# Kernel tuning notes

Hardware: AMD Instinct MI355X
Metric: run time of the kernel (lower is better)

## Reference

```python
import jax, jax.numpy as jnp
import numpy as np
from functools import partial

STRIDES = (8, 16, 32)
SIZES = ((80, 80), (40, 40), (20, 20))
NUM_CLASSES = 80
NMS_THR = 0.65
SCORE_THR = 0.01
MAX_DET = 100  # fixed-size NMS output (padded; validity = scores > 0)


def setup_inputs() -> dict:
    key = jax.random.key(0)
    ks = jax.random.split(key, 9)
    B = 32
    out = {}
    for i, (h, w) in enumerate(SIZES):
        out[f"cls{i}"] = jax.random.normal(ks[3 * i], (B, NUM_CLASSES, h, w), jnp.float32)
        out[f"reg{i}"] = jax.random.normal(ks[3 * i + 1], (B, 4, h, w), jnp.float32)
        out[f"obj{i}"] = jax.random.normal(ks[3 * i + 2], (B, 1, h, w), jnp.float32)
    return out


def _grid_points():
    # MlvlPointGenerator.grid_priors(with_stride=True), offset=0: (x, y, stride, stride)
    pts = []
    for (h, w), s in zip(SIZES, STRIDES):
        xs = jnp.arange(w, dtype=jnp.float32) * s
        ys = jnp.arange(h, dtype=jnp.float32) * s
        xx, yy = jnp.meshgrid(xs, ys)  # [h, w], x varies fastest -> matches NHWC flatten
        st = jnp.full((h * w,), float(s), jnp.float32)
        pts.append(jnp.stack([xx.ravel(), yy.ravel(), st, st], axis=-1))
    return jnp.concatenate(pts, axis=0)  # [A, 4]


def _flatten(t, c):
    # [N, C, H, W] -> [N, H*W, C]  (permute(0,2,3,1).reshape)
    return t.transpose(0, 2, 3, 1).reshape(t.shape[0], -1, c)


def _decode(points, reg):
    # YOLOXBBoxDecoder: center = pred_xy * stride + point, wh = exp(pred_wh) * stride
    stride = points[:, 2:]                       # [A, 2]
    xys = reg[..., :2] * stride + points[:, :2]  # [B, A, 2]
    whs = jnp.exp(reg[..., 2:]) * stride         # [B, A, 2]
    return jnp.concatenate([xys - whs * 0.5, xys + whs * 0.5], axis=-1)  # x1y1x2y2


def _iou_one_vs_all(b, boxes):
    # b: [4], boxes: [A, 4]
    tl = jnp.maximum(b[:2], boxes[:, :2])
    br = jnp.minimum(b[2:], boxes[:, 2:])
    wh = jnp.clip(br - tl, 0.0)
    inter = wh[:, 0] * wh[:, 1]
    a1 = (b[2] - b[0]) * (b[3] - b[1])
    a2 = (boxes[:, 2] - boxes[:, 0]) * (boxes[:, 3] - boxes[:, 1])
    return inter / (a1 + a2 - inter + 1e-6)


def _nms_image(boxes, cls_scores, objectness):
    # boxes [A,4], cls_scores [A,C] (post-sigmoid), objectness [A] (post-sigmoid)
    max_scores = jnp.max(cls_scores, axis=1)
    labels = jnp.argmax(cls_scores, axis=1)
    scores = max_scores * objectness
    live = jnp.where(scores >= SCORE_THR, scores, -jnp.inf)  # score_thr filter

    # batched_nms: offset boxes per class so boxes of different labels never overlap
    offset = jax.lax.stop_gradient(jnp.max(jnp.abs(boxes)) + 1.0)
    boxes_off = jax.lax.stop_gradient(boxes) + labels.astype(boxes.dtype)[:, None] * offset

    def body(i, state):
        live, keep, kscores = state
        best = jnp.argmax(live)
        kscores = kscores.at[i].set(live[best])
        keep = keep.at[i].set(best)
        iou = _iou_one_vs_all(boxes_off[best], boxes_off)
        live = jnp.where(iou > NMS_THR, -jnp.inf, live)
        live = live.at[best].set(-jnp.inf)
        return live, keep, kscores

    keep0 = jnp.zeros((MAX_DET,), jnp.int32)
    ks0 = jnp.full((MAX_DET,), -jnp.inf, boxes.dtype)
    _, keep, kscores = jax.lax.fori_loop(0, MAX_DET, body, (live, keep0, ks0))

    valid = kscores > -jnp.inf
    out_boxes = jnp.where(valid[:, None], boxes[keep], 0.0)
    out_scores = jnp.where(valid, scores[keep], 0.0)
    out_labels = jnp.where(valid, labels[keep], -1)
    return out_boxes, out_scores, out_labels, valid


def _forward(cls0, cls1, cls2, reg0, reg1, reg2, obj0, obj1, obj2):
    B = cls0.shape[0]
    flat_cls = jax.nn.sigmoid(jnp.concatenate([_flatten(c, NUM_CLASSES) for c in (cls0, cls1, cls2)], axis=1))
    flat_reg = jnp.concatenate([_flatten(r, 4) for r in (reg0, reg1, reg2)], axis=1)
    flat_obj = jax.nn.sigmoid(jnp.concatenate([_flatten(o, 1) for o in (obj0, obj1, obj2)], axis=1))[..., 0]
    points = _grid_points()
    boxes = _decode(points, flat_reg)  # [B, A, 4]
    return jax.vmap(_nms_image)(boxes, flat_cls, flat_obj)


@jax.jit
def reference(cls0, cls1, cls2, reg0, reg1, reg2, obj0, obj1, obj2):
    return _forward(cls0, cls1, cls2, reg0, reg1, reg2, obj0, obj1, obj2)
```

## Files before the change

kernel.cpp:

```cpp
#include <hip/hip_runtime.h>
#include <cmath>

typedef unsigned int uint;
typedef unsigned long long ull;

#define BATCH 32
#define NA 8400
#define NC 80
#define MAXDET 100
#define NMSTHR 0.65f
#define SCTHR 0.01f
#define NEG_INF (-INFINITY)

#define NT 1024
#define NW (NT / 64)
#define EPT 9
#define NBINS 4096
#define CAP 512

__device__ __forceinline__ float stable_sigmoid(float x) {
    if (x >= 0.f) return 1.f / (1.f + expf(-x));
    float e = expf(x);
    return e / (1.f + e);
}

template<int HW, int W, int S>
__device__ __forceinline__ void decode_one(
    const float* __restrict__ cls, const float* __restrict__ reg,
    const float* __restrict__ obj, int b, int p, size_t gidx,
    float4* __restrict__ wboxes, float* __restrict__ wscores, int* __restrict__ wlabels)
{
    const float* cbase = cls + (size_t)b * NC * HW + p;

    float mq[4]; int lq[4];
    #pragma unroll
    for (int q = 0; q < 4; ++q) { mq[q] = NEG_INF; lq[q] = 0; }
    #pragma unroll
    for (int q = 0; q < 4; ++q) {
        #pragma unroll
        for (int c2 = 0; c2 < 20; ++c2) {
            int c = q * 20 + c2;
            float v = cbase[(size_t)c * HW];
            if (v > mq[q]) { mq[q] = v; lq[q] = c; }
        }
    }
    float maxv = mq[0]; int lab = lq[0];
    #pragma unroll
    for (int q = 1; q < 4; ++q)
        if (mq[q] > maxv) { maxv = mq[q]; lab = lq[q]; }

    const float* rb = reg + (size_t)b * 4 * HW + p;
    float r0 = rb[0];
    float r1 = rb[HW];
    float r2 = rb[2 * (size_t)HW];
    float r3 = rb[3 * (size_t)HW];
    float ov = obj[(size_t)b * HW + p];

    int y = p / W;
    int x = p - y * W;
    float score = stable_sigmoid(maxv) * stable_sigmoid(ov);
    float cx = r0 * (float)S + (float)x * (float)S;
    float cy = r1 * (float)S + (float)y * (float)S;
    float bw = expf(r2) * (float)S;
    float bh = expf(r3) * (float)S;

    wboxes[gidx]  = make_float4(cx - bw * 0.5f, cy - bh * 0.5f,
                                cx + bw * 0.5f, cy + bh * 0.5f);
    wscores[gidx] = score;
    wlabels[gidx] = lab;
}

__global__ __launch_bounds__(256) void decode_kernel(
    const float* __restrict__ cls0, const float* __restrict__ reg0, const float* __restrict__ obj0,
    const float* __restrict__ cls1, const float* __restrict__ reg1, const float* __restrict__ obj1,
    const float* __restrict__ cls2, const float* __restrict__ reg2, const float* __restrict__ obj2,
    float4* __restrict__ wboxes, float* __restrict__ wscores, int* __restrict__ wlabels)
{
    int gid = blockIdx.x * blockDim.x + threadIdx.x;
    int b = gid / NA;
    int j = gid - b * NA;
    size_t gidx = (size_t)gid;

    if (j < 6400)
        decode_one<6400, 80, 8>(cls0, reg0, obj0, b, j, gidx, wboxes, wscores, wlabels);
    else if (j < 8000)
        decode_one<1600, 40, 16>(cls1, reg1, obj1, b, j - 6400, gidx, wboxes, wscores, wlabels);
    else
        decode_one<400, 20, 32>(cls2, reg2, obj2, b, j - 8000, gidx, wboxes, wscores, wlabels);
}

__global__ __launch_bounds__(NT) void nms_kernel(
    const float4* __restrict__ wboxes, const float* __restrict__ wscores,
    const int* __restrict__ wlabels, float* __restrict__ out)
{
    int b = blockIdx.x;
    int t = threadIdx.x;
    int lane = t & 63;
    int wv = t >> 6;
    const float4* boxes  = wboxes  + (size_t)b * NA;
    const float*  scores = wscores + (size_t)b * NA;
    const int*    labels = wlabels + (size_t)b * NA;

    __shared__ uint  s_keys[NA];
    __shared__ uint  s_hist[NBINS];
    __shared__ uint  s_cum[NBINS + 1];
    __shared__ uint  s_wsum[NW];
    __shared__ ull   s_skey[CAP];
    __shared__ float s_kbox[MAXDET][4];
    __shared__ float s_ka1[MAXDET];
    __shared__ int   s_kidx[MAXDET];
    __shared__ float s_kscr[MAXDET];
    __shared__ int   s_klab[MAXDET];
    __shared__ float s_red[NW];
    __shared__ float s_off;
    __shared__ int   s_kept, s_winlo, s_winhi, s_nsel;

    float m = 0.f;
    #pragma unroll
    for (int w = 0; w < EPT; ++w) {
        int e = t + w * NT;
        if (e < NA) {
            float4 v = boxes[e];
            m = fmaxf(m, fmaxf(fmaxf(fabsf(v.x), fabsf(v.y)),
                               fmaxf(fabsf(v.z), fabsf(v.w))));
        }
    }
    #pragma unroll
    for (int o = 32; o >= 1; o >>= 1) m = fmaxf(m, __shfl_xor(m, o));
    if (lane == 0) s_red[wv] = m;
    __syncthreads();
    if (t == 0) {
        float mm = 0.f;
        for (int w = 0; w < NW; ++w) mm = fmaxf(mm, s_red[w]);
        s_off = mm + 1.f;
        s_kept = 0;
        s_winlo = 0;
    }

    #pragma unroll
    for (int w = 0; w < EPT; ++w) {
        int e = t + w * NT;
        if (e < NA) {
            float sc = scores[e];
            s_keys[e] = (sc >= SCTHR) ? ~__float_as_uint(sc) : 0xFFFFFFFFu;
        }
    }
    for (int i = t; i < NBINS; i += NT) s_hist[i] = 0;
    __syncthreads();
    float off = s_off;
    #pragma unroll
    for (int w = 0; w < EPT; ++w) {
        int e = t + w * NT;
        if (e < NA) {
            uint k = s_keys[e];
            if (k != 0xFFFFFFFFu) atomicAdd(&s_hist[k >> 20], 1u);
        }
    }
    __syncthreads();

    uint l0 = s_hist[4 * t], l1 = s_hist[4 * t + 1],
         l2 = s_hist[4 * t + 2], l3 = s_hist[4 * t + 3];
    uint L = l0 + l1 + l2 + l3;
    uint ls = L;
    #pragma unroll
    for (int o = 1; o < 64; o <<= 1) {
        uint v = __shfl_up(ls, o);
        if (lane >= o) ls += v;
    }
    if (lane == 63) s_wsum[wv] = ls;
    __syncthreads();
    if (t < NW) {
        uint v = s_wsum[t];
        uint vs = v;
        #pragma unroll
        for (int o = 1; o < NW; o <<= 1) {
            uint u = __shfl_up(vs, o);
            if ((t & 63) >= o) vs += u;
        }
        s_wsum[t] = vs - v;
    }
    __syncthreads();
    uint base = s_wsum[wv] + (ls - L);
    s_cum[4 * t]     = base;
    s_cum[4 * t + 1] = base + l0;
    s_cum[4 * t + 2] = base + l0 + l1;
    s_cum[4 * t + 3] = base + l0 + l1 + l2;
    if (t == NT - 1) s_cum[NBINS] = base + L;

    for (;;) {
        __syncthreads();
        int kept = s_kept, winlo = s_winlo;
        uint remaining = s_cum[NBINS] - s_cum[winlo];
        if (kept >= MAXDET || winlo >= NBINS || remaining == 0u) break;
        if (t == 0) { s_winhi = winlo + 1; s_nsel = 0; }
        if (t < CAP) s_skey[t] = ~0ull;
        __syncthreads();
        uint cl = s_cum[winlo];
        #pragma unroll
        for (int q = 0; q < 4; ++q) {
            int i = t + q * NT;
            if (i >= winlo && i < NBINS && (s_cum[i + 1] - cl) <= (uint)CAP)
                atomicMax(&s_winhi, i + 1);
        }
        __syncthreads();
        int winhi = s_winhi;

        #pragma unroll
        for (int w = 0; w < EPT; ++w) {
            int e = t + w * NT;
            bool q = false;
            uint k = 0;
            if (e < NA) {
                k = s_keys[e];
                if (k != 0xFFFFFFFFu) {
                    int bin = (int)(k >> 20);
                    q = (bin >= winlo && bin < winhi);
                }
            }
            ull mask = __ballot(q);
            if (mask) {
                int leader = __ffsll(mask) - 1;
                int pbase = 0;
                if (lane == leader) pbase = atomicAdd(&s_nsel, __popcll(mask));
                pbase = __shfl(pbase, leader);
                if (q) {
                    int pos = pbase + __popcll(mask & ((1ull << lane) - 1ull));
                    if (pos < CAP) s_skey[pos] = ((ull)k << 32) | (uint)e;
                }
            }
        }
        __syncthreads();
        int nsel = s_nsel; if (nsel > CAP) nsel = CAP;

        for (int k2 = 2; k2 <= CAP; k2 <<= 1) {
            for (int j = k2 >> 1; j > 0; j >>= 1) {
                __syncthreads();
                if (t < CAP) {
                    int p = t ^ j;
                    if (p > t) {
                        ull a = s_skey[t], bb = s_skey[p];
                        bool up = ((t & k2) == 0);
                        if ((a > bb) == up) { s_skey[t] = bb; s_skey[p] = a; }
                    }
                }
            }
        }
        __syncthreads();

        if (t < 64) {
            int kept2 = s_kept;
            for (int cb = 0; cb < nsel && kept2 < MAXDET; cb += 64) {
                int ci = cb + lane;
                ull sk = (ci < nsel) ? s_skey[ci] : ~0ull;
                bool has = (sk != ~0ull);
                int idx = 0, lab = 0;
                float sc = 0.f, c0 = 0.f, c1 = 0.f, c2 = 0.f, c3 = 0.f, ca = 0.f;
                if (has) {
                    idx = (int)(sk & 0xFFFFFFFFull);
                    sc  = __uint_as_float(~(uint)(sk >> 32));
                    float4 rb = boxes[idx];
                    lab = labels[idx];
                    float lo = (float)lab * off;
                    c0 = rb.x + lo; c1 = rb.y + lo; c2 = rb.z + lo; c3 = rb.w + lo;
                    ca = (c2 - c0) * (c3 - c1);
                    for (int q = 0; q < kept2; ++q) {
                        float tlx = fmaxf(s_kbox[q][0], c0);
                        float tly = fmaxf(s_kbox[q][1], c1);
                        float brx = fminf(s_kbox[q][2], c2);
                        float bry = fminf(s_kbox[q][3], c3);
                        float ww = fmaxf(brx - tlx, 0.f);
                        float hh = fmaxf(bry - tly, 0.f);
                        float inter = ww * hh;
                        float iou = inter / (s_ka1[q] + ca - inter + 1e-6f);
                        if (iou > NMSTHR) { has = false; break; }
                    }
                }
                ull am = __ballot(has);
                while (am && kept2 < MAXDET) {
                    int f = __ffsll(am) - 1;
                    float f0 = __shfl(c0, f), f1 = __shfl(c1, f);
                    float f2 = __shfl(c2, f), f3 = __shfl(c3, f);
                    float fa = __shfl(ca, f);
                    int   fidx = __shfl(idx, f);
                    int   flab = __shfl(lab, f);
                    float fsc  = __shfl(sc, f);
                    if (lane == 0) {
                        s_kbox[kept2][0] = f0; s_kbox[kept2][1] = f1;
                        s_kbox[kept2][2] = f2; s_kbox[kept2][3] = f3;
                        s_ka1[kept2] = fa; s_kidx[kept2] = fidx;
                        s_kscr[kept2] = fsc; s_klab[kept2] = flab;
                    }
                    kept2++;
                    if (lane == f) has = false;
                    if (has) {
                        float tlx = fmaxf(f0, c0), tly = fmaxf(f1, c1);
                        float brx = fminf(f2, c2), bry = fminf(f3, c3);
                        float ww = fmaxf(brx - tlx, 0.f), hh = fmaxf(bry - tly, 0.f);
                        float inter = ww * hh;
                        float iou = inter / (fa + ca - inter + 1e-6f);
                        if (iou > NMSTHR) has = false;
                    }
                    am = __ballot(has);
                }
            }
            if (lane == 0) s_kept = kept2;
        }
        __syncthreads();
        if (t == 0) s_winlo = s_winhi;
    }
    __syncthreads();

    if (t < MAXDET) {
        int kept = s_kept;
        float4 obx = make_float4(0.f, 0.f, 0.f, 0.f);
        float osc = 0.f, olab = -1.f, oval = 0.f;
        if (t < kept) {
            int idx = s_kidx[t];
            obx  = boxes[idx];
            osc  = s_kscr[t];
            olab = (float)s_klab[t];
            oval = 1.f;
        }
        float* ob = out + ((size_t)b * MAXDET + t) * 4;
        ob[0] = obx.x; ob[1] = obx.y; ob[2] = obx.z; ob[3] = obx.w;
        out[BATCH * MAXDET * 4 + b * MAXDET + t] = osc;
        out[BATCH * MAXDET * 5 + b * MAXDET + t] = olab;
        out[BATCH * MAXDET * 6 + b * MAXDET + t] = oval;
    }
}

extern "C" void kernel_launch(void* const* d_in, const int* in_sizes, int n_in,
                              void* d_out, int out_size, void* d_ws, size_t ws_size,
                              hipStream_t stream) {
    const float* cls0 = (const float*)d_in[0];
    const float* reg0 = (const float*)d_in[1];
    const float* obj0 = (const float*)d_in[2];
    const float* cls1 = (const float*)d_in[3];
    const float* reg1 = (const float*)d_in[4];
    const float* obj1 = (const float*)d_in[5];
    const float* cls2 = (const float*)d_in[6];
    const float* reg2 = (const float*)d_in[7];
    const float* obj2 = (const float*)d_in[8];

    char* ws = (char*)d_ws;
    float4* wboxes  = (float4*)ws;
    float*  wscores = (float*)(ws + (size_t)BATCH * NA * sizeof(float4));
    int*    wlabels = (int*)(ws + (size_t)BATCH * NA * (sizeof(float4) + sizeof(float)));

    int total = BATCH * NA;
    decode_kernel<<<total / 256, 256, 0, stream>>>(
        cls0, reg0, obj0, cls1, reg1, obj1, cls2, reg2, obj2,
        wboxes, wscores, wlabels);

    nms_kernel<<<BATCH, NT, 0, stream>>>(wboxes, wscores, wlabels, (float*)d_out);
}
```

Measured before the change: 178.2 us.

## Move score keys, histogram and max-abs reduction into decode kernel; register bitonic sort

The decode kernel now also computes the sort keys, a per-image score histogram built with global atomics, and the per-image max absolute box coordinate. These three values were previously recomputed by a single 1024-thread block per image in the NMS kernel, whose prologue was a serial pass over 8400 boxes; moving them to the widely parallel decode kernel removes that pass. The bitonic sort now keeps keys in registers and uses wave shuffles for strides below 64, so block barriers are only needed for the larger strides. In exchange it adds a memset launch, contended global atomics on the histograms, and per-element global reads of the keys in the NMS selection loop.

```diff
diff --git a/kernel.cpp b/kernel.cpp
--- a/kernel.cpp
+++ b/kernel.cpp
@@ -27,8 +27,8 @@
 template<int HW, int W, int S>
 __device__ __forceinline__ void decode_one(
     const float* __restrict__ cls, const float* __restrict__ reg,
-    const float* __restrict__ obj, int b, int p, size_t gidx,
-    float4* __restrict__ wboxes, float* __restrict__ wscores, int* __restrict__ wlabels)
+    const float* __restrict__ obj, int b, int p,
+    float4* box, float* score, int* lab_out)
 {
     const float* cbase = cls + (size_t)b * NC * HW + p;
 
@@ -58,51 +58,72 @@
 
     int y = p / W;
     int x = p - y * W;
-    float score = stable_sigmoid(maxv) * stable_sigmoid(ov);
+    float sc = stable_sigmoid(maxv) * stable_sigmoid(ov);
     float cx = r0 * (float)S + (float)x * (float)S;
     float cy = r1 * (float)S + (float)y * (float)S;
     float bw = expf(r2) * (float)S;
     float bh = expf(r3) * (float)S;
 
-    wboxes[gidx]  = make_float4(cx - bw * 0.5f, cy - bh * 0.5f,
-                                cx + bw * 0.5f, cy + bh * 0.5f);
-    wscores[gidx] = score;
-    wlabels[gidx] = lab;
+    *box = make_float4(cx - bw * 0.5f, cy - bh * 0.5f,
+                       cx + bw * 0.5f, cy + bh * 0.5f);
+    *score = sc;
+    *lab_out = lab;
 }
 
 __global__ __launch_bounds__(256) void decode_kernel(
     const float* __restrict__ cls0, const float* __restrict__ reg0, const float* __restrict__ obj0,
     const float* __restrict__ cls1, const float* __restrict__ reg1, const float* __restrict__ obj1,
     const float* __restrict__ cls2, const float* __restrict__ reg2, const float* __restrict__ obj2,
-    float4* __restrict__ wboxes, float* __restrict__ wscores, int* __restrict__ wlabels)
+    float4* __restrict__ wboxes, int* __restrict__ wlabels, uint* __restrict__ wkeys,
+    uint* __restrict__ whist, uint* __restrict__ wmaxabs)
 {
     int gid = blockIdx.x * blockDim.x + threadIdx.x;
     int b = gid / NA;
     int j = gid - b * NA;
-    size_t gidx = (size_t)gid;
-
+    int lane = threadIdx.x & 63;
+
+    float4 box; float score; int lab;
     if (j < 6400)
-        decode_one<6400, 80, 8>(cls0, reg0, obj0, b, j, gidx, wboxes, wscores, wlabels);
+        decode_one<6400, 80, 8>(cls0, reg0, obj0, b, j, &box, &score, &lab);
     else if (j < 8000)
-        decode_one<1600, 40, 16>(cls1, reg1, obj1, b, j - 6400, gidx, wboxes, wscores, wlabels);
+        decode_one<1600, 40, 16>(cls1, reg1, obj1, b, j - 6400, &box, &score, &lab);
     else
-        decode_one<400, 20, 32>(cls2, reg2, obj2, b, j - 8000, gidx, wboxes, wscores, wlabels);
+        decode_one<400, 20, 32>(cls2, reg2, obj2, b, j - 8000, &box, &score, &lab);
+
+    wboxes[gid]  = box;
+    wlabels[gid] = lab;
+    uint key = (score >= SCTHR) ? ~__float_as_uint(score) : 0xFFFFFFFFu;
+    wkeys[gid] = key;
+    if (key != 0xFFFFFFFFu) atomicAdd(&whist[(size_t)b * NBINS + (key >> 20)], 1u);
+
+    float m = fmaxf(fmaxf(fabsf(box.x), fabsf(box.y)),
+                    fmaxf(fabsf(box.z), fabsf(box.w)));
+    int b0 = __shfl(b, 0);
+    float mh = (b == b0) ? m : 0.f;
+    float ml = (b == b0) ? 0.f : m;
+    #pragma unroll
+    for (int o = 32; o >= 1; o >>= 1) {
+        mh = fmaxf(mh, __shfl_xor(mh, o));
+        ml = fmaxf(ml, __shfl_xor(ml, o));
+    }
+    if (lane == 0) atomicMax(&wmaxabs[b0], __float_as_uint(mh));
+    int b63 = __shfl(b, 63);
+    if (lane == 63 && b63 != b0) atomicMax(&wmaxabs[b63], __float_as_uint(ml));
 }
 
 __global__ __launch_bounds__(NT) void nms_kernel(
-    const float4* __restrict__ wboxes, const float* __restrict__ wscores,
-    const int* __restrict__ wlabels, float* __restrict__ out)
+    const float4* __restrict__ wboxes, const int* __restrict__ wlabels,
+    const uint* __restrict__ wkeys, const uint* __restrict__ whist,
+    const uint* __restrict__ wmaxabs, float* __restrict__ out)
 {
     int b = blockIdx.x;
     int t = threadIdx.x;
     int lane = t & 63;
     int wv = t >> 6;
     const float4* boxes  = wboxes  + (size_t)b * NA;
-    const float*  scores = wscores + (size_t)b * NA;
     const int*    labels = wlabels + (size_t)b * NA;
-
-    __shared__ uint  s_keys[NA];
-    __shared__ uint  s_hist[NBINS];
+    const uint*   keys   = wkeys   + (size_t)b * NA;
+
     __shared__ uint  s_cum[NBINS + 1];
     __shared__ uint  s_wsum[NW];
     __shared__ ull   s_skey[CAP];
@@ -111,55 +132,12 @@
     __shared__ int   s_kidx[MAXDET];
     __shared__ float s_kscr[MAXDET];
     __shared__ int   s_klab[MAXDET];
-    __shared__ float s_red[NW];
-    __shared__ float s_off;
     __shared__ int   s_kept, s_winlo, s_winhi, s_nsel;
 
-    float m = 0.f;
-    #pragma unroll
-    for (int w = 0; w < EPT; ++w) {
-        int e = t + w * NT;
-        if (e < NA) {
-            float4 v = boxes[e];
-            m = fmaxf(m, fmaxf(fmaxf(fabsf(v.x), fabsf(v.y)),
-                               fmaxf(fabsf(v.z), fabsf(v.w))));
-        }
-    }
-    #pragma unroll
-    for (int o = 32; o >= 1; o >>= 1) m = fmaxf(m, __shfl_xor(m, o));
-    if (lane == 0) s_red[wv] = m;
-    __syncthreads();
-    if (t == 0) {
-        float mm = 0.f;
-        for (int w = 0; w < NW; ++w) mm = fmaxf(mm, s_red[w]);
-        s_off = mm + 1.f;
-        s_kept = 0;
-        s_winlo = 0;
-    }
-
-    #pragma unroll
-    for (int w = 0; w < EPT; ++w) {
-        int e = t + w * NT;
-        if (e < NA) {
-            float sc = scores[e];
-            s_keys[e] = (sc >= SCTHR) ? ~__float_as_uint(sc) : 0xFFFFFFFFu;
-        }
-    }
-    for (int i = t; i < NBINS; i += NT) s_hist[i] = 0;
-    __syncthreads();
-    float off = s_off;
-    #pragma unroll
-    for (int w = 0; w < EPT; ++w) {
-        int e = t + w * NT;
-        if (e < NA) {
-            uint k = s_keys[e];
-            if (k != 0xFFFFFFFFu) atomicAdd(&s_hist[k >> 20], 1u);
-        }
-    }
-    __syncthreads();
-
-    uint l0 = s_hist[4 * t], l1 = s_hist[4 * t + 1],
-         l2 = s_hist[4 * t + 2], l3 = s_hist[4 * t + 3];
+    float off = __uint_as_float(wmaxabs[b]) + 1.f;
+
+    uint4 h = ((const uint4*)(whist + (size_t)b * NBINS))[t];
+    uint l0 = h.x, l1 = h.y, l2 = h.z, l3 = h.w;
     uint L = l0 + l1 + l2 + l3;
     uint ls = L;
     #pragma unroll
@@ -168,6 +146,7 @@
         if (lane >= o) ls += v;
     }
     if (lane == 63) s_wsum[wv] = ls;
+    if (t == 0) { s_kept = 0; s_winlo = 0; }
     __syncthreads();
     if (t < NW) {
         uint v = s_wsum[t];
@@ -211,7 +190,7 @@
             bool q = false;
             uint k = 0;
             if (e < NA) {
-                k = s_keys[e];
+                k = keys[e];
                 if (k != 0xFFFFFFFFu) {
                     int bin = (int)(k >> 20);
                     q = (bin >= winlo && bin < winhi);
@@ -232,19 +211,28 @@
         __syncthreads();
         int nsel = s_nsel; if (nsel > CAP) nsel = CAP;
 
+        ull k = (t < CAP) ? s_skey[t] : ~0ull;
         for (int k2 = 2; k2 <= CAP; k2 <<= 1) {
             for (int j = k2 >> 1; j > 0; j >>= 1) {
-                __syncthreads();
-                if (t < CAP) {
-                    int p = t ^ j;
-                    if (p > t) {
-                        ull a = s_skey[t], bb = s_skey[p];
-                        bool up = ((t & k2) == 0);
-                        if ((a > bb) == up) { s_skey[t] = bb; s_skey[p] = a; }
+                if (j >= 64) {
+                    if (t < CAP) s_skey[t] = k;
+                    __syncthreads();
+                    if (t < CAP) {
+                        ull kp = s_skey[t ^ j];
+                        bool low = (t & j) == 0;
+                        bool up  = (t & k2) == 0;
+                        k = ((k < kp) == (low == up)) ? k : kp;
                     }
+                    __syncthreads();
+                } else if (t < CAP) {
+                    ull kp = __shfl_xor(k, j);
+                    bool low = (t & j) == 0;
+                    bool up  = (t & k2) == 0;
+                    k = ((k < kp) == (low == up)) ? k : kp;
                 }
             }
         }
+        if (t < CAP) s_skey[t] = k;
         __syncthreads();
 
         if (t < 64) {
@@ -343,14 +331,20 @@
     const float* obj2 = (const float*)d_in[8];
 
     char* ws = (char*)d_ws;
+    size_t nBA = (size_t)BATCH * NA;
     float4* wboxes  = (float4*)ws;
-    float*  wscores = (float*)(ws + (size_t)BATCH * NA * sizeof(float4));
-    int*    wlabels = (int*)(ws + (size_t)BATCH * NA * (sizeof(float4) + sizeof(float)));
+    int*    wlabels = (int*)(ws + nBA * 16);
+    uint*   wkeys   = (uint*)(ws + nBA * 20);
+    uint*   whist   = (uint*)(ws + nBA * 24);
+    uint*   wmaxabs = (uint*)(ws + nBA * 24 + (size_t)BATCH * NBINS * 4);
+
+    hipMemsetAsync(whist, 0, (size_t)BATCH * NBINS * 4 + BATCH * 4, stream);
 
     int total = BATCH * NA;
     decode_kernel<<<total / 256, 256, 0, stream>>>(
         cls0, reg0, obj0, cls1, reg1, obj1, cls2, reg2, obj2,
-        wboxes, wscores, wlabels);
-
-    nms_kernel<<<BATCH, NT, 0, stream>>>(wboxes, wscores, wlabels, (float*)d_out);
-}
+        wboxes, wlabels, wkeys, whist, wmaxabs);
+
+    nms_kernel<<<BATCH, NT, 0, stream>>>(wboxes, wlabels, wkeys, whist, wmaxabs,
+                                         (float*)d_out);
+}
```

After: 222.5 us. 24.9% more time.

## Split class argmax across 4 lanes, precompute sort keys, shuffle-based bitonic sort

Applied to the files above, without the earlier changes.

The decode kernel now assigns four threads per anchor. Each thread scans 20 classes and the partial maxima are merged with cross-lane shuffles, which raises parallelism and the number of memory loads in flight. Decode also writes the score-derived sort keys directly, so the NMS kernel no longer stages keys in shared memory and rereads them from global memory instead. The bitonic sort keeps keys in registers and uses wave shuffles for strides below 64, cutting barriers and shared-memory traffic. Tie handling in the argmax uses the lowest class index, which matches argmax semantics.

```diff
diff --git a/kernel.cpp b/kernel.cpp
--- a/kernel.cpp
+++ b/kernel.cpp
@@ -25,83 +25,83 @@
 }
 
 template<int HW, int W, int S>
-__device__ __forceinline__ void decode_one(
+__device__ __forceinline__ void decode4(
     const float* __restrict__ cls, const float* __restrict__ reg,
-    const float* __restrict__ obj, int b, int p, size_t gidx,
-    float4* __restrict__ wboxes, float* __restrict__ wscores, int* __restrict__ wlabels)
+    const float* __restrict__ obj, int b, int p, int q, int ag,
+    float4* __restrict__ wboxes, int* __restrict__ wlabels, uint* __restrict__ wkeys)
 {
-    const float* cbase = cls + (size_t)b * NC * HW + p;
-
-    float mq[4]; int lq[4];
-    #pragma unroll
-    for (int q = 0; q < 4; ++q) { mq[q] = NEG_INF; lq[q] = 0; }
-    #pragma unroll
-    for (int q = 0; q < 4; ++q) {
-        #pragma unroll
-        for (int c2 = 0; c2 < 20; ++c2) {
-            int c = q * 20 + c2;
-            float v = cbase[(size_t)c * HW];
-            if (v > mq[q]) { mq[q] = v; lq[q] = c; }
-        }
-    }
-    float maxv = mq[0]; int lab = lq[0];
-    #pragma unroll
-    for (int q = 1; q < 4; ++q)
-        if (mq[q] > maxv) { maxv = mq[q]; lab = lq[q]; }
-
-    const float* rb = reg + (size_t)b * 4 * HW + p;
-    float r0 = rb[0];
-    float r1 = rb[HW];
-    float r2 = rb[2 * (size_t)HW];
-    float r3 = rb[3 * (size_t)HW];
-    float ov = obj[(size_t)b * HW + p];
-
-    int y = p / W;
-    int x = p - y * W;
-    float score = stable_sigmoid(maxv) * stable_sigmoid(ov);
-    float cx = r0 * (float)S + (float)x * (float)S;
-    float cy = r1 * (float)S + (float)y * (float)S;
-    float bw = expf(r2) * (float)S;
-    float bh = expf(r3) * (float)S;
-
-    wboxes[gidx]  = make_float4(cx - bw * 0.5f, cy - bh * 0.5f,
-                                cx + bw * 0.5f, cy + bh * 0.5f);
-    wscores[gidx] = score;
-    wlabels[gidx] = lab;
+    const float* cbase = cls + (size_t)b * NC * HW + (size_t)(q * 20) * HW + p;
+    float v[20];
+    #pragma unroll
+    for (int i = 0; i < 20; ++i) v[i] = cbase[(size_t)i * HW];
+    float m = v[0]; int c = 0;
+    #pragma unroll
+    for (int i = 1; i < 20; ++i)
+        if (v[i] > m) { m = v[i]; c = i; }
+    c += q * 20;
+
+    #pragma unroll
+    for (int o = 1; o <= 2; o <<= 1) {
+        float om = __shfl_xor(m, o);
+        int   oc = __shfl_xor(c, o);
+        if (om > m || (om == m && oc < c)) { m = om; c = oc; }
+    }
+
+    if (q == 0) {
+        const float* rb = reg + (size_t)b * 4 * HW + p;
+        float r0 = rb[0];
+        float r1 = rb[HW];
+        float r2 = rb[2 * (size_t)HW];
+        float r3 = rb[3 * (size_t)HW];
+        float ov = obj[(size_t)b * HW + p];
+
+        int y = p / W;
+        int x = p - y * W;
+        float sc = stable_sigmoid(m) * stable_sigmoid(ov);
+        float cx = r0 * (float)S + (float)x * (float)S;
+        float cy = r1 * (float)S + (float)y * (float)S;
+        float bw = expf(r2) * (float)S;
+        float bh = expf(r3) * (float)S;
+
+        wboxes[ag]  = make_float4(cx - bw * 0.5f, cy - bh * 0.5f,
+                                  cx + bw * 0.5f, cy + bh * 0.5f);
+        wlabels[ag] = c;
+        wkeys[ag]   = (sc >= SCTHR) ? ~__float_as_uint(sc) : 0xFFFFFFFFu;
+    }
 }
 
 __global__ __launch_bounds__(256) void decode_kernel(
     const float* __restrict__ cls0, const float* __restrict__ reg0, const float* __restrict__ obj0,
     const float* __restrict__ cls1, const float* __restrict__ reg1, const float* __restrict__ obj1,
     const float* __restrict__ cls2, const float* __restrict__ reg2, const float* __restrict__ obj2,
-    float4* __restrict__ wboxes, float* __restrict__ wscores, int* __restrict__ wlabels)
+    float4* __restrict__ wboxes, int* __restrict__ wlabels, uint* __restrict__ wkeys)
 {
     int gid = blockIdx.x * blockDim.x + threadIdx.x;
-    int b = gid / NA;
-    int j = gid - b * NA;
-    size_t gidx = (size_t)gid;
+    int ag = gid >> 2;
+    int q  = gid & 3;
+    int b = ag / NA;
+    int j = ag - b * NA;
 
     if (j < 6400)
-        decode_one<6400, 80, 8>(cls0, reg0, obj0, b, j, gidx, wboxes, wscores, wlabels);
+        decode4<6400, 80, 8>(cls0, reg0, obj0, b, j, q, ag, wboxes, wlabels, wkeys);
     else if (j < 8000)
-        decode_one<1600, 40, 16>(cls1, reg1, obj1, b, j - 6400, gidx, wboxes, wscores, wlabels);
+        decode4<1600, 40, 16>(cls1, reg1, obj1, b, j - 6400, q, ag, wboxes, wlabels, wkeys);
     else
-        decode_one<400, 20, 32>(cls2, reg2, obj2, b, j - 8000, gidx, wboxes, wscores, wlabels);
+        decode4<400, 20, 32>(cls2, reg2, obj2, b, j - 8000, q, ag, wboxes, wlabels, wkeys);
 }
 
 __global__ __launch_bounds__(NT) void nms_kernel(
-    const float4* __restrict__ wboxes, const float* __restrict__ wscores,
-    const int* __restrict__ wlabels, float* __restrict__ out)
+    const float4* __restrict__ wboxes, const int* __restrict__ wlabels,
+    const uint* __restrict__ wkeys, float* __restrict__ out)
 {
     int b = blockIdx.x;
     int t = threadIdx.x;
     int lane = t & 63;
     int wv = t >> 6;
     const float4* boxes  = wboxes  + (size_t)b * NA;
-    const float*  scores = wscores + (size_t)b * NA;
     const int*    labels = wlabels + (size_t)b * NA;
-
-    __shared__ uint  s_keys[NA];
+    const uint*   keys   = wkeys   + (size_t)b * NA;
+
     __shared__ uint  s_hist[NBINS];
     __shared__ uint  s_cum[NBINS + 1];
     __shared__ uint  s_wsum[NW];
@@ -128,35 +128,24 @@
     #pragma unroll
     for (int o = 32; o >= 1; o >>= 1) m = fmaxf(m, __shfl_xor(m, o));
     if (lane == 0) s_red[wv] = m;
+    for (int i = t; i < NBINS; i += NT) s_hist[i] = 0;
+    if (t == 0) { s_kept = 0; s_winlo = 0; }
     __syncthreads();
     if (t == 0) {
         float mm = 0.f;
         for (int w = 0; w < NW; ++w) mm = fmaxf(mm, s_red[w]);
         s_off = mm + 1.f;
-        s_kept = 0;
-        s_winlo = 0;
-    }
-
+    }
     #pragma unroll
     for (int w = 0; w < EPT; ++w) {
         int e = t + w * NT;
         if (e < NA) {
-            float sc = scores[e];
-            s_keys[e] = (sc >= SCTHR) ? ~__float_as_uint(sc) : 0xFFFFFFFFu;
-        }
-    }
-    for (int i = t; i < NBINS; i += NT) s_hist[i] = 0;
+            uint k = keys[e];
+            if (k != 0xFFFFFFFFu) atomicAdd(&s_hist[k >> 20], 1u);
+        }
+    }
     __syncthreads();
     float off = s_off;
-    #pragma unroll
-    for (int w = 0; w < EPT; ++w) {
-        int e = t + w * NT;
-        if (e < NA) {
-            uint k = s_keys[e];
-            if (k != 0xFFFFFFFFu) atomicAdd(&s_hist[k >> 20], 1u);
-        }
-    }
-    __syncthreads();
 
     uint l0 = s_hist[4 * t], l1 = s_hist[4 * t + 1],
          l2 = s_hist[4 * t + 2], l3 = s_hist[4 * t + 3];
@@ -211,7 +200,7 @@
             bool q = false;
             uint k = 0;
             if (e < NA) {
-                k = s_keys[e];
+                k = keys[e];
                 if (k != 0xFFFFFFFFu) {
                     int bin = (int)(k >> 20);
                     q = (bin >= winlo && bin < winhi);
@@ -232,19 +221,28 @@
         __syncthreads();
         int nsel = s_nsel; if (nsel > CAP) nsel = CAP;
 
+        ull k = (t < CAP) ? s_skey[t] : ~0ull;
         for (int k2 = 2; k2 <= CAP; k2 <<= 1) {
             for (int j = k2 >> 1; j > 0; j >>= 1) {
-                __syncthreads();
-                if (t < CAP) {
-                    int p = t ^ j;
-                    if (p > t) {
-                        ull a = s_skey[t], bb = s_skey[p];
-                        bool up = ((t & k2) == 0);
-                        if ((a > bb) == up) { s_skey[t] = bb; s_skey[p] = a; }
+                if (j >= 64) {
+                    if (t < CAP) s_skey[t] = k;
+                    __syncthreads();
+                    if (t < CAP) {
+                        ull kp = s_skey[t ^ j];
+                        bool low = (t & j) == 0;
+                        bool up  = (t & k2) == 0;
+                        k = ((k < kp) == (low == up)) ? k : kp;
                     }
+                    __syncthreads();
+                } else if (t < CAP) {
+                    ull kp = __shfl_xor(k, j);
+                    bool low = (t & j) == 0;
+                    bool up  = (t & k2) == 0;
+                    k = ((k < kp) == (low == up)) ? k : kp;
                 }
             }
         }
+        if (t < CAP) s_skey[t] = k;
         __syncthreads();
 
         if (t < 64) {
@@ -343,14 +341,15 @@
     const float* obj2 = (const float*)d_in[8];
 
     char* ws = (char*)d_ws;
+    size_t nBA = (size_t)BATCH * NA;
     float4* wboxes  = (float4*)ws;
-    float*  wscores = (float*)(ws + (size_t)BATCH * NA * sizeof(float4));
-    int*    wlabels = (int*)(ws + (size_t)BATCH * NA * (sizeof(float4) + sizeof(float)));
-
-    int total = BATCH * NA;
+    int*    wlabels = (int*)(ws + nBA * 16);
+    uint*   wkeys   = (uint*)(ws + nBA * 20);
+
+    int total = BATCH * NA * 4;
     decode_kernel<<<total / 256, 256, 0, stream>>>(
         cls0, reg0, obj0, cls1, reg1, obj1, cls2, reg2, obj2,
-        wboxes, wscores, wlabels);
-
-    nms_kernel<<<BATCH, NT, 0, stream>>>(wboxes, wscores, wlabels, (float*)d_out);
-}
+        wboxes, wlabels, wkeys);
+
+    nms_kernel<<<BATCH, NT, 0, stream>>>(wboxes, wlabels, wkeys, (float*)d_out);
+}
```

Result: slower. 184.7 us (+3.7%).
